# Kernel tuning notes

Hardware: AMD Instinct MI355X
Metric: run time of the kernel (lower is better)

Reference implementation:

```python
import jax, jax.numpy as jnp
import numpy as np

# FlowNetC correlation hyperparameters (from init_kwargs)
PAD = 20
KS = 1
MD = 20
S1 = 1
S2 = 2
MUL = 1


def setup_inputs() -> dict:
    key = jax.random.key(0)
    k1, k2 = jax.random.split(key)
    B, C, H, W = 8, 256, 96, 128
    input1 = jax.random.normal(k1, (B, C, H, W), dtype=jnp.float32)
    input2 = jax.random.normal(k2, (B, C, H, W), dtype=jnp.float32)
    return {"input1": input1, "input2": input2}


def _correlation(in1, in2):
    b, c, h, w = in1.shape
    p1 = jnp.pad(in1, ((0, 0), (0, 0), (PAD, PAD), (PAD, PAD)))
    p2 = jnp.pad(in2, ((0, 0), (0, 0), (PAD, PAD), (PAD, PAD)))
    hp, wp = h + 2 * PAD, w + 2 * PAD
    out_h = (hp - 2 * MD - KS) // S1 + 1
    out_w = (wp - 2 * MD - KS) // S1 + 1
    d = 2 * MD // S2 + 1  # number of displacement steps per axis (21)

    # fixed center region of input1: [b, c, out_h, out_w]
    region1 = p1[:, :, MD:MD + out_h * S1:S1, MD:MD + out_w * S1:S1]

    offs = (jnp.arange(d) - d // 2) * S2  # displacement offsets
    dys, dxs = jnp.meshgrid(offs, offs, indexing='ij')
    dys = dys.reshape(-1)
    dxs = dxs.reshape(-1)

    def step(carry, dydx):
        dy, dx = dydx
        y0 = MD + dy
        x0 = MD + dx
        valid = (y0 >= 0) & (x0 >= 0) & (y0 + out_h * S1 <= hp) & (x0 + out_w * S1 <= wp)
        reg2 = jax.lax.dynamic_slice(
            p2, (0, 0, y0, x0), (b, c, out_h * S1, out_w * S1)
        )[:, :, ::S1, ::S1]
        corr = (region1 * reg2).sum(axis=1) * MUL  # [b, out_h, out_w]
        corr = jnp.where(valid, corr, jnp.zeros_like(corr))
        return carry, corr

    _, chans = jax.lax.scan(step, None, (dys, dxs))  # [d*d, b, out_h, out_w]
    return jnp.transpose(chans, (1, 0, 2, 3))  # [b, d*d, out_h, out_w]


def reference(input1, input2):
    return _correlation(input1, input2)
```

## Files before the change

kernel.cpp:

```cpp
#include <hip/hip_runtime.h>
#include <stdint.h>

#define B_N   8
#define C_N   256
#define H_N   96
#define W_N   128
#define NCK   8
#define ND    21
#define NK    (ND * ND)

typedef __attribute__((ext_vector_type(8))) short short8;
typedef __attribute__((ext_vector_type(4))) float f32x4;

__device__ char zchunk[12288];

__device__ __forceinline__ uint32_t f2bf(float f) {
  uint32_t u = __builtin_bit_cast(uint32_t, f);
  return (u + 0x7fffu + ((u >> 16) & 1u)) >> 16;
}
__device__ __forceinline__ uint32_t packbf(float lo, float hi) {
  return f2bf(lo) | (f2bf(hi) << 16);
}

__global__ __launch_bounds__(256) void prep(const float* __restrict__ in1,
                                            const float* __restrict__ in2,
                                            unsigned short* __restrict__ Apre,
                                            unsigned short* __restrict__ Bpre) {
  __shared__ float tile[32][W_N + 1];
  int blk = blockIdx.x;
  bool isA = blk < 6144;
  int rblk = isA ? blk : blk - 6144;
  int ck = rblk & 7, bi = rblk >> 3;
  int b = bi / H_N, row = bi % H_N;
  const float* src = (isA ? in1 : in2) + ((size_t)(b * C_N + ck * 32) * H_N + row) * W_N;
  int tid = threadIdx.x;
  for (int idx = tid; idx < 32 * W_N; idx += 256) {
    int c = idx >> 7, j = idx & 127;
    tile[c][j] = src[(size_t)c * (H_N * W_N) + j];
  }
  __syncthreads();
  if (isA) {
    uint32_t* dst = (uint32_t*)Apre + (size_t)rblk * 2048;
    for (int q = tid; q < 2048; q += 256) {
      int e2 = q & 3, ln = (q >> 2) & 63, tp = q >> 8;
      int t = tp >> 1, p = tp & 1;
      int m = ln & 15, kg = ln >> 4;
      int c0 = kg * 8 + 2 * e2;
      int j = 32 * t + 2 * m + p;
      dst[q] = packbf(tile[c0][j], tile[c0 + 1][j]);
    }
  } else {
    uint32_t* dst = (uint32_t*)Bpre + (size_t)rblk * 3072;
    for (int q = tid; q < 3072; q += 256) {
      int e2 = q & 3, ln = (q >> 2) & 63, sp = q >> 8;
      int s = sp >> 1, p = sp & 1;
      int m = ln & 15, kg = ln >> 4;
      int c0 = kg * 8 + 2 * e2;
      int x = 32 * s + 2 * m - 20 + p;
      dst[q] = ((unsigned)x < 128u) ? packbf(tile[c0][x], tile[c0 + 1][x]) : 0u;
    }
  }
}

__global__ __launch_bounds__(256, 3) void corr_main(const unsigned short* __restrict__ Apre,
                                                    const unsigned short* __restrict__ Bpre,
                                                    float* __restrict__ out) {
  __shared__ float outl[ND][W_N + 1];

  int h = blockIdx.x;
  int l = (h & 7) * 672 + (h >> 3);
  int c = l / 7, q = l - 7 * c;
  int b = c / 96, i0 = c - 96 * b;
  int gidx = 6 - q;
  int i = i0 + 6 * q; if (i >= H_N) i -= H_N;
  int bi = b * H_N + i;
  int dyb = gidx * 3;

  int tid = threadIdx.x;
  int lane = tid & 63, w = tid >> 6;
  int p = w & 1, th = w >> 1;
  int m = lane & 15, kg = lane >> 4;

  f32x4 acc[2][3][3];
#pragma unroll
  for (int a0i = 0; a0i < 2; ++a0i)
#pragma unroll
    for (int a1i = 0; a1i < 3; ++a1i)
#pragma unroll
      for (int a2i = 0; a2i < 3; ++a2i) acc[a0i][a1i][a2i] = {0.f, 0.f, 0.f, 0.f};

  const char* Ap = (const char*)Apre + (size_t)bi * 65536
                   + (((4 * th + p)) << 10) + lane * 16;
  const char* Bp[3];
  int bstr[3];
#pragma unroll
  for (int g = 0; g < 3; ++g) {
    int y = i + 2 * (dyb + g) - 20;
    bool v = (unsigned)y < (unsigned)H_N;
    const char* base = v ? (const char*)Bpre + (size_t)(b * H_N + y) * 98304
                         : (const char*)zchunk;
    Bp[g] = base + ((4 * th + p) << 10) + lane * 16;
    bstr[g] = v ? 12288 : 0;
  }

#pragma unroll 2
  for (int ck = 0; ck < NCK; ++ck) {
    short8 a0 = *(const short8*)(Ap);
    short8 a1 = *(const short8*)(Ap + 2048);
    short8 bb[4][3];
#pragma unroll
    for (int ss = 0; ss < 4; ++ss)
#pragma unroll
      for (int g = 0; g < 3; ++g)
        bb[ss][g] = *(const short8*)(Bp[g] + ss * 2048);
#pragma unroll
    for (int ss = 0; ss < 4; ++ss)
#pragma unroll
      for (int g = 0; g < 3; ++g) {
        if (ss <= 2) acc[0][g][ss]     = __builtin_amdgcn_mfma_f32_16x16x32_bf16(a0, bb[ss][g], acc[0][g][ss], 0, 0, 0);
        if (ss >= 1) acc[1][g][ss - 1] = __builtin_amdgcn_mfma_f32_16x16x32_bf16(a1, bb[ss][g], acc[1][g][ss - 1], 0, 0, 0);
      }
    Ap += 8192;
    Bp[0] += bstr[0]; Bp[1] += bstr[1]; Bp[2] += bstr[2];
  }

#pragma unroll
  for (int g = 0; g < 3; ++g) {
    __syncthreads();
#pragma unroll
    for (int tt = 0; tt < 2; ++tt) {
      int t = 2 * th + tt;
#pragma unroll
      for (int dl = 0; dl < 3; ++dl) {
#pragma unroll
        for (int r = 0; r < 4; ++r) {
          int a_ = kg * 4 + r;
          int dxi = 16 * dl + m - a_;
          if (dxi >= 0 && dxi <= 20) {
            int j = 2 * (16 * t + a_) + p;
            outl[dxi][j] = acc[tt][g][dl][r];
          }
        }
      }
    }
    __syncthreads();
    int dyi = dyb + g;
    size_t obase = ((size_t)(b * NK + dyi * ND) * H_N + i) * W_N;
    for (int idx = tid; idx < ND * W_N; idx += 256) {
      int dxi = idx >> 7, j = idx & 127;
      out[obase + (size_t)dxi * (H_N * W_N) + j] = outl[dxi][j];
    }
  }
}

__global__ void corr_naive(const float* __restrict__ in1, const float* __restrict__ in2,
                           float* __restrict__ out) {
  size_t o = (size_t)blockIdx.x * 256 + threadIdx.x;
  const size_t total = (size_t)B_N * NK * H_N * W_N;
  if (o >= total) return;
  int j = o & 127;
  int i = (int)((o >> 7) % H_N);
  int k = (int)((o / ((size_t)H_N * W_N)) % NK);
  int b = (int)(o / ((size_t)NK * H_N * W_N));
  int dyi = k / ND, dxi = k % ND;
  int y = i + 2 * dyi - 20, x = j + 2 * dxi - 20;
  float s = 0.f;
  if ((unsigned)y < (unsigned)H_N && (unsigned)x < (unsigned)W_N) {
    const float* p1 = in1 + ((size_t)b * C_N * H_N + i) * W_N + j;
    const float* p2 = in2 + ((size_t)b * C_N * H_N + y) * W_N + x;
    for (int c = 0; c < C_N; ++c)
      s += p1[(size_t)c * H_N * W_N] * p2[(size_t)c * H_N * W_N];
  }
  out[o] = s;
}

extern "C" void kernel_launch(void* const* d_in, const int* in_sizes, int n_in,
                              void* d_out, int out_size, void* d_ws, size_t ws_size,
                              hipStream_t stream) {
  const float* in1 = (const float*)d_in[0];
  const float* in2 = (const float*)d_in[1];
  float* out = (float*)d_out;

  const size_t A_BYTES = (size_t)6144 * 8192;
  const size_t B_BYTES = (size_t)6144 * 12288;
  if (ws_size < A_BYTES + B_BYTES) {
    size_t total = (size_t)B_N * NK * H_N * W_N;
    corr_naive<<<(int)((total + 255) / 256), 256, 0, stream>>>(in1, in2, out);
    return;
  }
  unsigned short* Apre = (unsigned short*)d_ws;
  unsigned short* Bpre = (unsigned short*)((char*)d_ws + A_BYTES);

  prep<<<12288, 256, 0, stream>>>(in1, in2, Apre, Bpre);
  corr_main<<<5376, 256, 0, stream>>>(Apre, Bpre, out);
}
```

Measured before the change: 208.3 us.

## Restructure correlation MFMA tiling with triangular block sharing and double-buffered fragment loads

Changes each wave's work from two column tiles by three shift tiles to a triangular set of six tile pairs, loading three A and three B fragments per channel chunk. The second wave half swaps operand order so it computes the transposed block. The channel loop is fully unrolled into a double-buffered load/compute sequence separated by sched_barrier. Launch bounds drop to one block per SM minimum, which allows more registers but may lower occupancy.

Measured after the change: 208.1 us. About the same (-0.1%).

```diff
diff --git a/kernel.cpp b/kernel.cpp
--- a/kernel.cpp
+++ b/kernel.cpp
@@ -62,7 +62,53 @@
   }
 }
 
-__global__ __launch_bounds__(256, 3) void corr_main(const unsigned short* __restrict__ Apre,
+#define DECL_FRAGS(F) short8 F##_a0, F##_a1, F##_a2, \
+                             F##_b00, F##_b01, F##_b02, \
+                             F##_b10, F##_b11, F##_b12, \
+                             F##_b20, F##_b21, F##_b22
+
+#define LOADF(F, CK) do {                                                        \
+  F##_a0  = *(const short8*)(Ap  + (size_t)(CK) * 8192);                         \
+  F##_a1  = *(const short8*)(Ap  + (size_t)(CK) * 8192 + 2048);                  \
+  F##_a2  = *(const short8*)(Ap  + (size_t)(CK) * 8192 + 4096);                  \
+  F##_b00 = *(const short8*)(Bp0 + (size_t)(CK) * bstr0);                        \
+  F##_b01 = *(const short8*)(Bp0 + (size_t)(CK) * bstr0 + 2048);                 \
+  F##_b02 = *(const short8*)(Bp0 + (size_t)(CK) * bstr0 + 4096);                 \
+  F##_b10 = *(const short8*)(Bp1 + (size_t)(CK) * bstr1);                        \
+  F##_b11 = *(const short8*)(Bp1 + (size_t)(CK) * bstr1 + 2048);                 \
+  F##_b12 = *(const short8*)(Bp1 + (size_t)(CK) * bstr1 + 4096);                 \
+  F##_b20 = *(const short8*)(Bp2 + (size_t)(CK) * bstr2);                        \
+  F##_b21 = *(const short8*)(Bp2 + (size_t)(CK) * bstr2 + 2048);                 \
+  F##_b22 = *(const short8*)(Bp2 + (size_t)(CK) * bstr2 + 4096);                 \
+} while (0)
+
+#define MF(a, b, c) __builtin_amdgcn_mfma_f32_16x16x32_bf16(a, b, c, 0, 0, 0)
+
+#define COMPG0(F, G) do {                                                        \
+  acc[G][0] = MF(F##_a0, F##_b##G##0, acc[G][0]);                                \
+  acc[G][1] = MF(F##_a0, F##_b##G##1, acc[G][1]);                                \
+  acc[G][2] = MF(F##_a1, F##_b##G##1, acc[G][2]);                                \
+  acc[G][3] = MF(F##_a0, F##_b##G##2, acc[G][3]);                                \
+  acc[G][4] = MF(F##_a1, F##_b##G##2, acc[G][4]);                                \
+  acc[G][5] = MF(F##_a2, F##_b##G##2, acc[G][5]);                                \
+} while (0)
+#define COMPG1(F, G) do {                                                        \
+  acc[G][0] = MF(F##_b##G##0, F##_a0, acc[G][0]);                                \
+  acc[G][1] = MF(F##_b##G##0, F##_a1, acc[G][1]);                                \
+  acc[G][2] = MF(F##_b##G##1, F##_a1, acc[G][2]);                                \
+  acc[G][3] = MF(F##_b##G##0, F##_a2, acc[G][3]);                                \
+  acc[G][4] = MF(F##_b##G##1, F##_a2, acc[G][4]);                                \
+  acc[G][5] = MF(F##_b##G##2, F##_a2, acc[G][5]);                                \
+} while (0)
+
+#define COMPUTE(F) do {                                                          \
+  if (th == 0) { COMPG0(F, 0); COMPG0(F, 1); COMPG0(F, 2); }                     \
+  else         { COMPG1(F, 0); COMPG1(F, 1); COMPG1(F, 2); }                     \
+} while (0)
+
+#define SB() __builtin_amdgcn_sched_barrier(0)
+
+__global__ __launch_bounds__(256, 1) void corr_main(const unsigned short* __restrict__ Apre,
                                                     const unsigned short* __restrict__ Bpre,
                                                     float* __restrict__ out) {
   __shared__ float outl[ND][W_N + 1];
@@ -81,64 +127,64 @@
   int p = w & 1, th = w >> 1;
   int m = lane & 15, kg = lane >> 4;
 
-  f32x4 acc[2][3][3];
-#pragma unroll
-  for (int a0i = 0; a0i < 2; ++a0i)
-#pragma unroll
-    for (int a1i = 0; a1i < 3; ++a1i)
-#pragma unroll
-      for (int a2i = 0; a2i < 3; ++a2i) acc[a0i][a1i][a2i] = {0.f, 0.f, 0.f, 0.f};
+  f32x4 acc[3][6];
+#pragma unroll
+  for (int gi = 0; gi < 3; ++gi)
+#pragma unroll
+    for (int ki = 0; ki < 6; ++ki) acc[gi][ki] = {0.f, 0.f, 0.f, 0.f};
 
   const char* Ap = (const char*)Apre + (size_t)bi * 65536
-                   + (((4 * th + p)) << 10) + lane * 16;
-  const char* Bp[3];
-  int bstr[3];
-#pragma unroll
-  for (int g = 0; g < 3; ++g) {
-    int y = i + 2 * (dyb + g) - 20;
-    bool v = (unsigned)y < (unsigned)H_N;
-    const char* base = v ? (const char*)Bpre + (size_t)(b * H_N + y) * 98304
-                         : (const char*)zchunk;
-    Bp[g] = base + ((4 * th + p) << 10) + lane * 16;
-    bstr[g] = v ? 12288 : 0;
-  }
-
-#pragma unroll 2
-  for (int ck = 0; ck < NCK; ++ck) {
-    short8 a0 = *(const short8*)(Ap);
-    short8 a1 = *(const short8*)(Ap + 2048);
-    short8 bb[4][3];
-#pragma unroll
-    for (int ss = 0; ss < 4; ++ss)
-#pragma unroll
-      for (int g = 0; g < 3; ++g)
-        bb[ss][g] = *(const short8*)(Bp[g] + ss * 2048);
-#pragma unroll
-    for (int ss = 0; ss < 4; ++ss)
-#pragma unroll
-      for (int g = 0; g < 3; ++g) {
-        if (ss <= 2) acc[0][g][ss]     = __builtin_amdgcn_mfma_f32_16x16x32_bf16(a0, bb[ss][g], acc[0][g][ss], 0, 0, 0);
-        if (ss >= 1) acc[1][g][ss - 1] = __builtin_amdgcn_mfma_f32_16x16x32_bf16(a1, bb[ss][g], acc[1][g][ss - 1], 0, 0, 0);
-      }
-    Ap += 8192;
-    Bp[0] += bstr[0]; Bp[1] += bstr[1]; Bp[2] += bstr[2];
-  }
+                   + th * 2048 + p * 1024 + lane * 16;
+  const char* Bp0; const char* Bp1; const char* Bp2;
+  int bstr0, bstr1, bstr2;
+  {
+    int y0 = i + 2 * dyb - 20;
+#pragma unroll
+    for (int g = 0; g < 3; ++g) {
+      int y = y0 + 2 * g;
+      bool v = (unsigned)y < (unsigned)H_N;
+      const char* base = v ? (const char*)Bpre + (size_t)(b * H_N + y) * 98304
+                           : (const char*)zchunk;
+      const char* bp = base + th * 6144 + p * 1024 + lane * 16;
+      int bs = v ? 12288 : 0;
+      if (g == 0) { Bp0 = bp; bstr0 = bs; }
+      else if (g == 1) { Bp1 = bp; bstr1 = bs; }
+      else { Bp2 = bp; bstr2 = bs; }
+    }
+  }
+
+  DECL_FRAGS(fA);
+  DECL_FRAGS(fB);
+
+  LOADF(fA, 0);
+  LOADF(fB, 1);
+  SB();
+  COMPUTE(fA); LOADF(fA, 2); SB();
+  COMPUTE(fB); LOADF(fB, 3); SB();
+  COMPUTE(fA); LOADF(fA, 4); SB();
+  COMPUTE(fB); LOADF(fB, 5); SB();
+  COMPUTE(fA); LOADF(fA, 6); SB();
+  COMPUTE(fB); LOADF(fB, 7); SB();
+  COMPUTE(fA); SB();
+  COMPUTE(fB);
 
 #pragma unroll
   for (int g = 0; g < 3; ++g) {
     __syncthreads();
-#pragma unroll
-    for (int tt = 0; tt < 2; ++tt) {
-      int t = 2 * th + tt;
-#pragma unroll
-      for (int dl = 0; dl < 3; ++dl) {
+    {
+      const int T0c[6] = {0, 0, 1, 0, 1, 2}, S0c[6] = {0, 1, 1, 2, 2, 2};
+      const int T1c[6] = {1, 2, 2, 3, 3, 3}, S1c[6] = {3, 3, 4, 3, 4, 5};
+#pragma unroll
+      for (int k = 0; k < 6; ++k) {
+        int T = th ? T1c[k] : T0c[k];
+        int S = th ? S1c[k] : S0c[k];
 #pragma unroll
         for (int r = 0; r < 4; ++r) {
           int a_ = kg * 4 + r;
-          int dxi = 16 * dl + m - a_;
+          int dxi = 16 * (S - T) + (th ? (a_ - m) : (m - a_));
           if (dxi >= 0 && dxi <= 20) {
-            int j = 2 * (16 * t + a_) + p;
-            outl[dxi][j] = acc[tt][g][dl][r];
+            int j = 2 * (16 * T + (th ? m : a_)) + p;
+            outl[dxi][j] = acc[g][k][r];
           }
         }
       }
```
